# Kernel tuning notes

Measured on AMD Instinct MI355X. Metric: run time of the kernel, lower is better.

## Reference

```python
import jax, jax.numpy as jnp
import numpy as np

B, P, K = 32, 2048, 20   # events, points per event, kNN neighbors
EPS = 1e-5               # BatchNorm eps (eval mode, running stats)


def setup_inputs() -> dict:
    key = jax.random.key(0)
    ks = iter(jax.random.split(key, 64))
    inp = {}
    inp["x"] = jax.random.normal(next(ks), (B * P, 7), jnp.float32)
    inp["batch"] = jnp.repeat(jnp.arange(B, dtype=jnp.int32), P)

    def add_layer(tag, cin, cout):
        inp["w" + tag] = jax.random.normal(next(ks), (cin, cout), jnp.float32) / np.sqrt(cin)
        inp["b" + tag] = jax.random.normal(next(ks), (cout,), jnp.float32) * 0.01
        inp["g" + tag] = jax.random.uniform(next(ks), (cout,), jnp.float32, 0.5, 1.5)
        inp["e" + tag] = jax.random.normal(next(ks), (cout,), jnp.float32) * 0.1
        inp["m" + tag] = jax.random.normal(next(ks), (cout,), jnp.float32) * 0.1
        inp["v" + tag] = jax.random.uniform(next(ks), (cout,), jnp.float32, 0.5, 1.5)

    # conv1 MLP: [14, 64, 64, 64]
    add_layer("10", 14, 64)
    add_layer("11", 64, 64)
    add_layer("12", 64, 64)
    # conv2 MLP: [128, 128]
    add_layer("20", 128, 128)
    return inp


def _lin_relu_bn(h, W, b, g, be, rm, rv):
    # Linear -> ReLU -> BatchNorm1d (eval mode: running stats)
    h = jax.nn.relu(h @ W + b)
    return (h - rm) * (g / jnp.sqrt(rv + EPS)) + be


def _knn_idx(x):
    # x: [B, P, C] -> indices of K nearest neighbors (incl. self), [B, P, K]
    sq = jnp.sum(x * x, axis=-1)                                   # [B, P]
    d = sq[:, :, None] + sq[:, None, :] - 2.0 * jnp.einsum("bpc,bqc->bpq", x, x)
    _, idx = jax.lax.top_k(-d, K)
    return idx


def _edge_conv(x, mlp):
    # DynamicEdgeConv: kNN graph on current features, edge MLP([x_i, x_j - x_i]), max-aggr
    idx = _knn_idx(x)                                              # [B, P, K]
    xj = jax.vmap(lambda xb, ib: xb[ib])(x, idx)                   # [B, P, K, C]
    xi = jnp.broadcast_to(x[:, :, None, :], xj.shape)
    e = jnp.concatenate([xi, xj - xi], axis=-1)                    # [B, P, K, 2C]
    return jnp.max(mlp(e), axis=2)                                 # [B, P, Cout]


def reference(x, batch,
              w10, b10, g10, e10, m10, v10,
              w11, b11, g11, e11, m11, v11,
              w12, b12, g12, e12, m12, v12,
              w20, b20, g20, e20, m20, v20):
    xb = x.reshape(B, P, -1)                                       # fixed-size events

    def mlp1(e):
        h = _lin_relu_bn(e, w10, b10, g10, e10, m10, v10)
        h = _lin_relu_bn(h, w11, b11, g11, e11, m11, v11)
        return _lin_relu_bn(h, w12, b12, g12, e12, m12, v12)

    def mlp2(e):
        return _lin_relu_bn(e, w20, b20, g20, e20, m20, v20)

    x1 = _edge_conv(xb, mlp1)                                      # [B, P, 64]
    x2 = _edge_conv(x1, mlp2)                                      # [B, P, 128]
    out = jnp.concatenate([x1, x2], axis=-1).reshape(B * P, 192)
    return out, batch
```

## Files before the change

kernel.cpp:

```cpp
#include <hip/hip_runtime.h>

#define B_EV 32
#define P_PT 2048
#define K_NN 20
#define NPTS (B_EV*P_PT)
#define EPS_BN 1e-5f
#define RINF 3.0e38f

typedef _Float16 half8 __attribute__((ext_vector_type(8)));
typedef float f32x4 __attribute__((ext_vector_type(4)));

static constexpr int oWA10=0, oWB10=448, oB10=896, oT10=960,
  oT11=5184,
  oT12=9408,
  oWA20=9472, oWB20=17664, oB20=25856, oT20=25984,
  oB11p=26048, oB12p=26112,
  oW11hi=26176, oW11lo=28224,
  oW12hi=30272, oW12lo=32320;
static constexpr size_t oIDX = 36864;
static constexpr size_t oA1  = 1347584;
static constexpr size_t oB1  = oA1 + (size_t)NPTS*64;
static constexpr size_t oV2  = oB1 + (size_t)NPTS*64;
static constexpr size_t oX1  = oV2 + (size_t)NPTS*128;
static constexpr size_t oSQ  = oX1 + (size_t)NPTS*64;
static constexpr size_t oD   = oSQ + (size_t)NPTS;
static constexpr size_t oU2  = oA1;

__global__ __launch_bounds__(128) void k_prep(
  const float* w10,const float* b10,const float* g10,const float* e10,const float* m10,const float* v10,
  const float* w11,const float* b11,const float* g11,const float* e11,const float* m11,const float* v11,
  const float* w12,const float* b12,const float* g12,const float* e12,const float* m12,const float* v12,
  const float* w20,const float* b20,const float* g20,const float* e20,const float* m20,const float* v20,
  float* ws)
{
  __shared__ float t10s[64], t11s[64];
  int c = threadIdx.x;
  if (c < 64) {
    float s0 = g10[c]*rsqrtf(v10[c]+EPS_BN);
    ws[oB10+c]=b10[c]*s0;
    float t10 = e10[c]-m10[c]*s0; ws[oT10+c]=t10; t10s[c]=t10;
    for (int i=0;i<7;i++){
      ws[oWA10+i*64+c]=(w10[i*64+c]-w10[(7+i)*64+c])*s0;
      ws[oWB10+i*64+c]=w10[(7+i)*64+c]*s0;
    }
    float s1 = g11[c]*rsqrtf(v11[c]+EPS_BN);
    float t11 = e11[c]-m11[c]*s1; ws[oT11+c]=t11; t11s[c]=t11;
    float s2 = g12[c]*rsqrtf(v12[c]+EPS_BN);
    ws[oT12+c]=e12[c]-m12[c]*s2;
  }
  __syncthreads();
  if (c < 64) {
    float s1 = g11[c]*rsqrtf(v11[c]+EPS_BN);
    _Float16* W1hi = (_Float16*)(ws + oW11hi);
    _Float16* W1lo = (_Float16*)(ws + oW11lo);
    float acc = b11[c]*s1;
    for (int i=0;i<64;i++){
      float wv = w11[i*64+c]*s1;
      _Float16 h = (_Float16)wv;
      W1hi[c*64+i] = h;
      W1lo[c*64+i] = (_Float16)(wv - (float)h);
      acc = fmaf(t10s[i], wv, acc);
    }
    ws[oB11p+c]=acc;
    float s2 = g12[c]*rsqrtf(v12[c]+EPS_BN);
    _Float16* W2hi = (_Float16*)(ws + oW12hi);
    _Float16* W2lo = (_Float16*)(ws + oW12lo);
    float acc2 = b12[c]*s2;
    for (int i=0;i<64;i++){
      float wv = w12[i*64+c]*s2;
      _Float16 h = (_Float16)wv;
      W2hi[c*64+i] = h;
      W2lo[c*64+i] = (_Float16)(wv - (float)h);
      acc2 = fmaf(t11s[i], wv, acc2);
    }
    ws[oB12p+c]=acc2;
  }
  {
    float s = g20[c]*rsqrtf(v20[c]+EPS_BN);
    ws[oB20+c]=b20[c]*s; ws[oT20+c]=e20[c]-m20[c]*s;
    for (int i=0;i<64;i++){
      ws[oWA20+i*128+c]=(w20[i*128+c]-w20[(64+i)*128+c])*s;
      ws[oWB20+i*128+c]=w20[(64+i)*128+c]*s;
    }
  }
}

__device__ __forceinline__ void select20(float (&d)[32], int lane, int base, int g,
                                         int* __restrict__ idxout)
{
  float g4[4];
  #pragma unroll
  for (int k=0;k<4;k++){
    float m = d[8*k];
    #pragma unroll
    for (int j=1;j<8;j++) m = fminf(m, d[8*k+j]);
    g4[k]=m;
  }
  float T = 0.f;
  #pragma unroll 1
  for (int pass=0; pass<20; ++pass){
    float m = fminf(fminf(g4[0],g4[1]), fminf(g4[2],g4[3]));
    #pragma unroll
    for (int off=32; off>0; off>>=1) m = fminf(m, __shfl_xor(m, off, 64));
    if (pass==19){ T=m; break; }
    #pragma unroll
    for (int k=0;k<4;k++){
      if (g4[k]==m){
        #pragma unroll
        for (int j=0;j<8;j++) d[8*k+j] = (d[8*k+j]==m) ? RINF : d[8*k+j];
        float mm = d[8*k];
        #pragma unroll
        for (int j=1;j<8;j++) mm = fminf(mm, d[8*k+j]);
        g4[k]=mm;
      }
    }
  }
  int cnt=0;
  #pragma unroll
  for (int j=0;j<32;j++){
    bool take = (d[j]>=RINF) || (d[j]==T);
    unsigned long long mb = __ballot(take);
    if (take){
      int pos = cnt + (int)__popcll(mb & ((1ull<<lane)-1ull));
      if (pos < K_NN) idxout[(size_t)g*K_NN + pos] = base + j*64 + lane;
    }
    cnt += (int)__popcll(mb);
  }
  if (lane==0){
    for (int r=cnt; r<K_NN; ++r) idxout[(size_t)g*K_NN + r] = g;
  }
}

__global__ __launch_bounds__(1024, 8) void k_knn1(const float* __restrict__ x, int* __restrict__ idxout)
{
  __shared__ float xs[P_PT*8];
  int t = threadIdx.x;
  int b = blockIdx.x;
  int xcd = b & 7, kk = b >> 3;
  int e = xcd + ((kk >> 7) << 3);
  int blk = kk & 127;
  {
    const float* xe = x + (size_t)e*P_PT*7;
    #pragma unroll
    for (int u=0; u<2; u++){
      int p = t + u*1024;
      float v0=xe[p*7+0], v1=xe[p*7+1], v2=xe[p*7+2], v3=xe[p*7+3];
      float v4=xe[p*7+4], v5=xe[p*7+5], v6=xe[p*7+6];
      int s = (p&7)<<2;
      int w0 = (p*8) ^ s;
      int w1 = (p*8+4) ^ s;
      f32x4 lo = {v0,v1,v2,v3};
      f32x4 hi = {v4,v5,v6,0.f};
      *(f32x4*)(xs + w0) = lo;
      *(f32x4*)(xs + w1) = hi;
    }
  }
  __syncthreads();
  int lane = t & 63;
  int g = e*P_PT + blk*16 + (t>>6);
  int pin = g & (P_PT-1);
  float xp[7];
  {
    int s = (pin&7)<<2;
    f32x4 lo = *(const f32x4*)(xs + ((pin*8)^s));
    f32x4 hi = *(const f32x4*)(xs + ((pin*8+4)^s));
    xp[0]=lo[0]; xp[1]=lo[1]; xp[2]=lo[2]; xp[3]=lo[3];
    xp[4]=hi[0]; xp[5]=hi[1]; xp[6]=hi[2];
  }
  int sl = (lane&7)<<2;
  const float* base0 = xs + ((lane*8)^sl);
  const float* base1 = xs + ((lane*8+4)^sl);
  float d[32];
  #pragma unroll
  for (int j=0;j<32;j++){
    f32x4 lo = *(const f32x4*)(base0 + j*512);
    f32x4 hi = *(const f32x4*)(base1 + j*512);
    float s=0.f, df;
    df = xp[0]-lo[0]; s=fmaf(df,df,s);
    df = xp[1]-lo[1]; s=fmaf(df,df,s);
    df = xp[2]-lo[2]; s=fmaf(df,df,s);
    df = xp[3]-lo[3]; s=fmaf(df,df,s);
    df = xp[4]-hi[0]; s=fmaf(df,df,s);
    df = xp[5]-hi[1]; s=fmaf(df,df,s);
    df = xp[6]-hi[2]; s=fmaf(df,df,s);
    d[j]=s;
  }
  select20(d, lane, e*P_PT, g, idxout);
}

__global__ __launch_bounds__(256) void k_ab1(const float* __restrict__ x, const float* __restrict__ W,
                                             float* __restrict__ A1, float* __restrict__ B1)
{
  int g = blockIdx.x*256+threadIdx.x;
  float xi[7];
  #pragma unroll
  for (int i=0;i<7;i++) xi[i]=x[(size_t)g*7+i];
  float a[64], b[64];
  #pragma unroll
  for (int c=0;c<64;c++){ a[c]=W[oB10+c]; b[c]=0.f; }
  #pragma unroll
  for (int i=0;i<7;i++){
    #pragma unroll
    for (int c=0;c<64;c++) a[c]=fmaf(xi[i], W[oWA10+i*64+c], a[c]);
    #pragma unroll
    for (int c=0;c<64;c++) b[c]=fmaf(xi[i], W[oWB10+i*64+c], b[c]);
  }
  #pragma unroll
  for (int c=0;c<64;c+=4){
    float4 oa; oa.x=a[c]; oa.y=a[c+1]; oa.z=a[c+2]; oa.w=a[c+3];
    *(float4*)(A1+(size_t)g*64+c)=oa;
    float4 ob; ob.x=b[c]; ob.y=b[c+1]; ob.z=b[c+2]; ob.w=b[c+3];
    *(float4*)(B1+(size_t)g*64+c)=ob;
  }
}

__global__ __launch_bounds__(256, 2) void k_ec1m(const int* __restrict__ idx, const float* __restrict__ ws,
    const float* __restrict__ A1, const float* __restrict__ B1,
    float* __restrict__ x1, float* __restrict__ sqv, float* __restrict__ out)
{
  __shared__ float h2s[4][48*64];
  int t = threadIdx.x, w = t>>6, lane = t&63;
  int b = blockIdx.x;
  int xcd = b & 7, kk = b >> 3;
  int ev = xcd + ((kk >> 8) << 3);
  int iA = ev*P_PT + (kk & 255)*8 + w*2;
  int iB = iA + 1;
  int lg = lane>>4, lr = lane&15;

  int jT0 = idx[(size_t)iA*K_NN + lr];
  int jT1 = idx[(size_t)iB*K_NN + lr];
  int a2 = (lr < 4) ? iA*K_NN + 16 + lr : iB*K_NN + 12 + lr;
  a2 = (lr < 8) ? a2 : 0;
  int jT2 = (lr < 8) ? idx[a2] : iA;

  const float* ApA = A1 + (size_t)iA*64;
  const float* ApB = A1 + (size_t)iB*64;
  float4 avA[2][2], avB[2][2], bv[3][2][2];
  const float* Bp0 = B1 + (size_t)jT0*64;
  const float* Bp1 = B1 + (size_t)jT1*64;
  const float* Bp2 = B1 + (size_t)jT2*64;
  #pragma unroll
  for (int ks=0;ks<2;ks++){
    int c0 = ks*32 + lg*8;
    avA[ks][0] = *(const float4*)(ApA+c0); avA[ks][1] = *(const float4*)(ApA+c0+4);
    avB[ks][0] = *(const float4*)(ApB+c0); avB[ks][1] = *(const float4*)(ApB+c0+4);
    bv[0][ks][0] = *(const float4*)(Bp0+c0); bv[0][ks][1] = *(const float4*)(Bp0+c0+4);
    bv[1][ks][0] = *(const float4*)(Bp1+c0); bv[1][ks][1] = *(const float4*)(Bp1+c0+4);
    bv[2][ks][0] = *(const float4*)(Bp2+c0); bv[2][ks][1] = *(const float4*)(Bp2+c0+4);
  }

  bool useB2 = (lr >= 4) && (lr < 8);
  half8 AH[3][2], AL[3][2];
  #pragma unroll
  for (int tile=0;tile<3;tile++){
    #pragma unroll
    for (int ks=0;ks<2;ks++){
      float4 a0, a1;
      if (tile==0){ a0 = avA[ks][0]; a1 = avA[ks][1]; }
      else if (tile==1){ a0 = avB[ks][0]; a1 = avB[ks][1]; }
      else {
        a0.x = useB2 ? avB[ks][0].x : avA[ks][0].x;  a0.y = useB2 ? avB[ks][0].y : avA[ks][0].y;
        a0.z = useB2 ? avB[ks][0].z : avA[ks][0].z;  a0.w = useB2 ? avB[ks][0].w : avA[ks][0].w;
        a1.x = useB2 ? avB[ks][1].x : avA[ks][1].x;  a1.y = useB2 ? avB[ks][1].y : avA[ks][1].y;
        a1.z = useB2 ? avB[ks][1].z : avA[ks][1].z;  a1.w = useB2 ? avB[ks][1].w : avA[ks][1].w;
      }
      float hv[8];
      hv[0]=fmaxf(a0.x+bv[tile][ks][0].x,0.f); hv[1]=fmaxf(a0.y+bv[tile][ks][0].y,0.f);
      hv[2]=fmaxf(a0.z+bv[tile][ks][0].z,0.f); hv[3]=fmaxf(a0.w+bv[tile][ks][0].w,0.f);
      hv[4]=fmaxf(a1.x+bv[tile][ks][1].x,0.f); hv[5]=fmaxf(a1.y+bv[tile][ks][1].y,0.f);
      hv[6]=fmaxf(a1.z+bv[tile][ks][1].z,0.f); hv[7]=fmaxf(a1.w+bv[tile][ks][1].w,0.f);
      half8 ah, al;
      #pragma unroll
      for (int q=0;q<8;q++){
        _Float16 h = (_Float16)hv[q];
        ah[q]=h; al[q]=(_Float16)(hv[q]-(float)h);
      }
      AH[tile][ks]=ah; AL[tile][ks]=al;
    }
  }

  f32x4 acc[3][4];
  #pragma unroll
  for (int nt=0;nt<4;nt++){
    float bb = ws[oB11p + nt*16 + lr];
    f32x4 v = {bb,bb,bb,bb};
    acc[0][nt]=v; acc[1][nt]=v; acc[2][nt]=v;
  }
  {
    const _Float16* W1hi = (const _Float16*)(ws + oW11hi);
    const _Float16* W1lo = (const _Float16*)(ws + oW11lo);
    #pragma unroll
    for (int nt=0;nt<4;nt++){
      const _Float16* whp = W1hi + (nt*16+lr)*64 + lg*8;
      const _Float16* wlp = W1lo + (nt*16+lr)*64 + lg*8;
      half8 wh0 = *(const half8*)(whp);
      half8 wh1 = *(const half8*)(whp+32);
      half8 wl0 = *(const half8*)(wlp);
      half8 wl1 = *(const half8*)(wlp+32);
      #pragma unroll
      for (int tile=0;tile<3;tile++){
        acc[tile][nt] = __builtin_amdgcn_mfma_f32_16x16x32_f16(AH[tile][0], wh0, acc[tile][nt], 0,0,0);
        acc[tile][nt] = __builtin_amdgcn_mfma_f32_16x16x32_f16(AL[tile][0], wh0, acc[tile][nt], 0,0,0);
        acc[tile][nt] = __builtin_amdgcn_mfma_f32_16x16x32_f16(AH[tile][0], wl0, acc[tile][nt], 0,0,0);
        acc[tile][nt] = __builtin_amdgcn_mfma_f32_16x16x32_f16(AH[tile][1], wh1, acc[tile][nt], 0,0,0);
        acc[tile][nt] = __builtin_amdgcn_mfma_f32_16x16x32_f16(AL[tile][1], wh1, acc[tile][nt], 0,0,0);
        acc[tile][nt] = __builtin_amdgcn_mfma_f32_16x16x32_f16(AH[tile][1], wl1, acc[tile][nt], 0,0,0);
      }
    }
  }

  float* hb = h2s[w];
  #pragma unroll
  for (int tile=0;tile<3;tile++){
    #pragma unroll
    for (int nt=0;nt<4;nt++){
      #pragma unroll
      for (int r=0;r<4;r++){
        int row = tile*16 + lg*4 + r;
        int col = nt*16 + lr;
        int baddr = (row*256 + col*4) ^ ((row&7)<<4);
        *(float*)((char*)hb + baddr) = fmaxf(acc[tile][nt][r], 0.f);
      }
    }
  }

  half8 AH2[3][2], AL2[3][2];
  #pragma unroll
  for (int tile=0;tile<3;tile++){
    #pragma unroll
    for (int ks=0;ks<2;ks++){
      int row = tile*16 + lr;
      int byte0 = (row*256 + (ks*32 + lg*8)*4);
      int s = (row&7)<<4;
      f32x4 v0 = *(const f32x4*)((char*)hb + ((byte0)^s));
      f32x4 v1 = *(const f32x4*)((char*)hb + ((byte0+16)^s));
      half8 ah, al;
      #pragma unroll
      for (int q=0;q<4;q++){
        _Float16 h = (_Float16)v0[q];
        ah[q]=h; al[q]=(_Float16)(v0[q]-(float)h);
      }
      #pragma unroll
      for (int q=0;q<4;q++){
        _Float16 h = (_Float16)v1[q];
        ah[4+q]=h; al[4+q]=(_Float16)(v1[q]-(float)h);
      }
      AH2[tile][ks]=ah; AL2[tile][ks]=al;
    }
  }

  f32x4 acc2[3][4];
  #pragma unroll
  for (int nt=0;nt<4;nt++){
    float bb = ws[oB12p + nt*16 + lr];
    f32x4 v = {bb,bb,bb,bb};
    acc2[0][nt]=v; acc2[1][nt]=v; acc2[2][nt]=v;
  }
  {
    const _Float16* W2hi = (const _Float16*)(ws + oW12hi);
    const _Float16* W2lo = (const _Float16*)(ws + oW12lo);
    #pragma unroll
    for (int nt=0;nt<4;nt++){
      const _Float16* whp = W2hi + (nt*16+lr)*64 + lg*8;
      const _Float16* wlp = W2lo + (nt*16+lr)*64 + lg*8;
      half8 wh0 = *(const half8*)(whp);
      half8 wh1 = *(const half8*)(whp+32);
      half8 wl0 = *(const half8*)(wlp);
      half8 wl1 = *(const half8*)(wlp+32);
      #pragma unroll
      for (int tile=0;tile<3;tile++){
        acc2[tile][nt] = __builtin_amdgcn_mfma_f32_16x16x32_f16(AH2[tile][0], wh0, acc2[tile][nt], 0,0,0);
        acc2[tile][nt] = __builtin_amdgcn_mfma_f32_16x16x32_f16(AL2[tile][0], wh0, acc2[tile][nt], 0,0,0);
        acc2[tile][nt] = __builtin_amdgcn_mfma_f32_16x16x32_f16(AH2[tile][0], wl0, acc2[tile][nt], 0,0,0);
        acc2[tile][nt] = __builtin_amdgcn_mfma_f32_16x16x32_f16(AH2[tile][1], wh1, acc2[tile][nt], 0,0,0);
        acc2[tile][nt] = __builtin_amdgcn_mfma_f32_16x16x32_f16(AL2[tile][1], wh1, acc2[tile][nt], 0,0,0);
        acc2[tile][nt] = __builtin_amdgcn_mfma_f32_16x16x32_f16(AH2[tile][1], wl1, acc2[tile][nt], 0,0,0);
      }
    }
  }

  float finA[4], finB[4];
  float sqA = 0.f, sqB = 0.f;
  #pragma unroll
  for (int nt=0;nt<4;nt++){
    float cvA = -RINF;
    #pragma unroll
    for (int r=0;r<4;r++) cvA = fmaxf(cvA, acc2[0][nt][r]);
    if (lg==0){
      #pragma unroll
      for (int r=0;r<4;r++) cvA = fmaxf(cvA, acc2[2][nt][r]);
    }
    cvA = fmaxf(cvA, __shfl_xor(cvA,16,64));
    cvA = fmaxf(cvA, __shfl_xor(cvA,32,64));
    finA[nt] = fmaxf(cvA, 0.f) + ws[oT12 + nt*16 + lr];
    sqA = fmaf(finA[nt], finA[nt], sqA);

    float cvB = -RINF;
    #pragma unroll
    for (int r=0;r<4;r++) cvB = fmaxf(cvB, acc2[1][nt][r]);
    if (lg==1){
      #pragma unroll
      for (int r=0;r<4;r++) cvB = fmaxf(cvB, acc2[2][nt][r]);
    }
    cvB = fmaxf(cvB, __shfl_xor(cvB,16,64));
    cvB = fmaxf(cvB, __shfl_xor(cvB,32,64));
    finB[nt] = fmaxf(cvB, 0.f) + ws[oT12 + nt*16 + lr];
    sqB = fmaf(finB[nt], finB[nt], sqB);
  }
  if (lane < 16){
    #pragma unroll
    for (int nt=0;nt<4;nt++){
      x1[(size_t)iA*64 + nt*16 + lane] = finA[nt];
      out[(size_t)iA*192 + nt*16 + lane] = finA[nt];
      x1[(size_t)iB*64 + nt*16 + lane] = finB[nt];
      out[(size_t)iB*192 + nt*16 + lane] = finB[nt];
    }
  }
  #pragma unroll
  for (int off=1; off<16; off<<=1){
    sqA += __shfl_xor(sqA, off, 64);
    sqB += __shfl_xor(sqB, off, 64);
  }
  if (lane == 0){ sqv[iA] = sqA; sqv[iB] = sqB; }
}

__global__ __launch_bounds__(256) void k_dist2(const float* __restrict__ x1, const float* __restrict__ sqv,
                                               float* __restrict__ D, int e0, int ce)
{
  __shared__ float As[64][68], Bs[64][68];
  int b = blockIdx.x;
  int z, inner;
  if (ce == 8){ z = b & 7; inner = b >> 3; }
  else        { z = b / 1024; inner = b % 1024; }
  int by = inner >> 5, bx = inner & 31;
  int e = e0 + z;
  const float* Xe = x1 + (size_t)e*P_PT*64;
  int rb = by*64, cb = bx*64;
  int t = threadIdx.x;
  int tr = t>>4, tk=(t&15)*4;
  #pragma unroll
  for (int rr=0;rr<4;rr++){
    int r = tr + 16*rr;
    float4 va = *(const float4*)(Xe + (size_t)(rb+r)*64 + tk);
    As[tk][r]=va.x; As[tk+1][r]=va.y; As[tk+2][r]=va.z; As[tk+3][r]=va.w;
    float4 vb = *(const float4*)(Xe + (size_t)(cb+r)*64 + tk);
    Bs[tk][r]=vb.x; Bs[tk+1][r]=vb.y; Bs[tk+2][r]=vb.z; Bs[tk+3][r]=vb.w;
  }
  __syncthreads();
  int tx=t&15, ty=t>>4;
  float acc[4][4];
  #pragma unroll
  for (int i=0;i<4;i++){
    #pragma unroll
    for (int j=0;j<4;j++) acc[i][j]=0.f;
  }
  #pragma unroll 4
  for (int k=0;k<64;k++){
    float4 a4 = *(const float4*)(&As[k][ty*4]);
    float4 b4 = *(const float4*)(&Bs[k][tx*4]);
    float a0=a4.x, a1=a4.y, a2=a4.z, a3=a4.w;
    float b0=b4.x, b1=b4.y, b2=b4.z, b3=b4.w;
    acc[0][0]=fmaf(a0,b0,acc[0][0]); acc[0][1]=fmaf(a0,b1,acc[0][1]);
    acc[0][2]=fmaf(a0,b2,acc[0][2]); acc[0][3]=fmaf(a0,b3,acc[0][3]);
    acc[1][0]=fmaf(a1,b0,acc[1][0]); acc[1][1]=fmaf(a1,b1,acc[1][1]);
    acc[1][2]=fmaf(a1,b2,acc[1][2]); acc[1][3]=fmaf(a1,b3,acc[1][3]);
    acc[2][0]=fmaf(a2,b0,acc[2][0]); acc[2][1]=fmaf(a2,b1,acc[2][1]);
    acc[2][2]=fmaf(a2,b2,acc[2][2]); acc[2][3]=fmaf(a2,b3,acc[2][3]);
    acc[3][0]=fmaf(a3,b0,acc[3][0]); acc[3][1]=fmaf(a3,b1,acc[3][1]);
    acc[3][2]=fmaf(a3,b2,acc[3][2]); acc[3][3]=fmaf(a3,b3,acc[3][3]);
  }
  float sr[4], sc[4];
  #pragma unroll
  for (int i=0;i<4;i++){ sr[i]=sqv[e*P_PT + rb+ty*4+i]; sc[i]=sqv[e*P_PT + cb+tx*4+i]; }
  #pragma unroll
  for (int i=0;i<4;i++){
    float4 o;
    o.x = sr[i]+sc[0]-2.f*acc[i][0];
    o.y = sr[i]+sc[1]-2.f*acc[i][1];
    o.z = sr[i]+sc[2]-2.f*acc[i][2];
    o.w = sr[i]+sc[3]-2.f*acc[i][3];
    *(float4*)(D + (size_t)(z*P_PT + rb+ty*4+i)*P_PT + cb + tx*4) = o;
  }
}

__global__ __launch_bounds__(256) void k_sel2(const float* __restrict__ D, int* __restrict__ idxout, int e0)
{
  int t=threadIdx.x, lane=t&63;
  int pl = blockIdx.x*4 + (t>>6);
  int le = pl>>11, pin = pl&(P_PT-1);
  int e = e0 + le;
  int g = e*P_PT + pin;
  const float* Dr = D + (size_t)pl*P_PT;
  float d[32];
  #pragma unroll
  for (int j=0;j<32;j++) d[j]=Dr[j*64+lane];
  select20(d, lane, e*P_PT, g, idxout);
}

__global__ __launch_bounds__(256) void k_uv2(const float* __restrict__ x1, const float* __restrict__ W,
                                             float* __restrict__ U2, float* __restrict__ V2)
{
  int g = blockIdx.x*256 + threadIdx.x;
  int half = blockIdx.y & 1;
  bool isU = blockIdx.y < 2;
  const float* Wb = W + (isU?oWA20:oWB20) + half*64;
  float acc[64];
  #pragma unroll
  for (int c=0;c<64;c++) acc[c] = isU ? W[oB20+half*64+c] : 0.f;
  const float* xp = x1 + (size_t)g*64;
  #pragma unroll 1
  for (int i=0;i<64;i+=4){
    float4 xv = *(const float4*)(xp+i);
    #pragma unroll
    for (int c=0;c<64;c++) acc[c]=fmaf(xv.x, Wb[(i+0)*128+c], acc[c]);
    #pragma unroll
    for (int c=0;c<64;c++) acc[c]=fmaf(xv.y, Wb[(i+1)*128+c], acc[c]);
    #pragma unroll
    for (int c=0;c<64;c++) acc[c]=fmaf(xv.z, Wb[(i+2)*128+c], acc[c]);
    #pragma unroll
    for (int c=0;c<64;c++) acc[c]=fmaf(xv.w, Wb[(i+3)*128+c], acc[c]);
  }
  float* dst = (isU?U2:V2) + (size_t)g*128 + half*64;
  #pragma unroll
  for (int c=0;c<64;c+=4){
    float4 o; o.x=acc[c]; o.y=acc[c+1]; o.z=acc[c+2]; o.w=acc[c+3];
    *(float4*)(dst+c)=o;
  }
}

__global__ __launch_bounds__(256) void k_gather2(const int* __restrict__ idx, const float* __restrict__ U2,
     const float* __restrict__ V2, const float* __restrict__ W, float* __restrict__ out)
{
  int b = blockIdx.x;
  int xcd = b & 7, kk = b >> 3;
  int ev = xcd + ((kk >> 3) << 3);
  int g = ev*P_PT + (kk & 7)*256 + threadIdx.x;
  int half = blockIdx.y;
  float mx[64];
  #pragma unroll
  for (int c=0;c<64;c++) mx[c]=-RINF;
  for (int k=0;k<K_NN;k++){
    int j = idx[(size_t)g*K_NN+k];
    const float4* vp = (const float4*)(V2 + (size_t)j*128 + half*64);
    #pragma unroll
    for (int c4=0;c4<16;c4++){
      float4 v=vp[c4];
      mx[c4*4+0]=fmaxf(mx[c4*4+0],v.x);
      mx[c4*4+1]=fmaxf(mx[c4*4+1],v.y);
      mx[c4*4+2]=fmaxf(mx[c4*4+2],v.z);
      mx[c4*4+3]=fmaxf(mx[c4*4+3],v.w);
    }
  }
  const float* Up = U2 + (size_t)g*128 + half*64;
  float* op = out + (size_t)g*192 + 64 + half*64;
  #pragma unroll
  for (int c=0;c<64;c+=4){
    float4 o;
    o.x = fmaxf(Up[c+0]+mx[c+0],0.f)+W[oT20+half*64+c+0];
    o.y = fmaxf(Up[c+1]+mx[c+1],0.f)+W[oT20+half*64+c+1];
    o.z = fmaxf(Up[c+2]+mx[c+2],0.f)+W[oT20+half*64+c+2];
    o.w = fmaxf(Up[c+3]+mx[c+3],0.f)+W[oT20+half*64+c+3];
    *(float4*)(op+c)=o;
  }
}

__global__ __launch_bounds__(256) void k_batchf(const int* __restrict__ batch, float* __restrict__ out){
  int i = blockIdx.x*256+threadIdx.x;
  out[(size_t)NPTS*192 + i] = (float)batch[i];
}

extern "C" void kernel_launch(void* const* d_in, const int* in_sizes, int n_in,
                              void* d_out, int out_size, void* d_ws, size_t ws_size,
                              hipStream_t stream)
{
  const float* x     = (const float*)d_in[0];
  const int*   batch = (const int*)d_in[1];
  const float* w10=(const float*)d_in[2],  *b10=(const float*)d_in[3],  *g10=(const float*)d_in[4],
             *e10=(const float*)d_in[5],  *m10=(const float*)d_in[6],  *v10=(const float*)d_in[7];
  const float* w11=(const float*)d_in[8],  *b11=(const float*)d_in[9],  *g11=(const float*)d_in[10],
             *e11=(const float*)d_in[11], *m11=(const float*)d_in[12], *v11=(const float*)d_in[13];
  const float* w12=(const float*)d_in[14], *b12=(const float*)d_in[15], *g12=(const float*)d_in[16],
             *e12=(const float*)d_in[17], *m12=(const float*)d_in[18], *v12=(const float*)d_in[19];
  const float* w20=(const float*)d_in[20], *b20=(const float*)d_in[21], *g20=(const float*)d_in[22],
             *e20=(const float*)d_in[23], *m20=(const float*)d_in[24], *v20=(const float*)d_in[25];

  float* ws  = (float*)d_ws;
  float* out = (float*)d_out;
  int*   idxp = (int*)(ws + oIDX);

  k_prep<<<1,128,0,stream>>>(w10,b10,g10,e10,m10,v10, w11,b11,g11,e11,m11,v11,
                             w12,b12,g12,e12,m12,v12, w20,b20,g20,e20,m20,v20, ws);
  k_knn1<<<NPTS/16, 1024, 0, stream>>>(x, idxp);
  k_ab1<<<NPTS/256, 256, 0, stream>>>(x, ws, ws+oA1, ws+oB1);
  k_ec1m<<<NPTS/8, 256, 0, stream>>>(idxp, ws, ws+oA1, ws+oB1, ws+oX1, ws+oSQ, out);

  size_t wsFloats = ws_size/4;
  long avail = (long)wsFloats - (long)oD;
  int CE = (int)(avail / (2048L*2048L));
  if (CE < 1) CE = 1;
  if (CE > 8) CE = 8;
  for (int e0=0; e0<B_EV; e0+=CE){
    int ce = (B_EV - e0 < CE) ? (B_EV - e0) : CE;
    k_dist2<<<ce*1024,256,0,stream>>>(ws+oX1, ws+oSQ, ws+oD, e0, ce);
    k_sel2<<<ce*512,256,0,stream>>>(ws+oD, idxp, e0);
  }

  k_uv2<<<dim3(NPTS/256,4),256,0,stream>>>(ws+oX1, ws, ws+oU2, ws+oV2);
  k_gather2<<<dim3(NPTS/256,2),256,0,stream>>>(idxp, ws+oU2, ws+oV2, ws, out);
  k_batchf<<<NPTS/256,256,0,stream>>>(batch, out);
}
```

Measured before the change: 1.002 ms.

## Fuse second-stage kNN distance and top-k selection into one MFMA kernel

Replaces the chunked k_dist2/k_sel2 pair, which wrote full 2048x2048 distance matrices per event to global memory and read them back, with one fused kernel. Each block computes distances for 16 query points against all points of the event using f16 MFMA, with a hi/lo split (four MFMAs) to recover near-fp32 accuracy, stages tiles through shared memory and selects top-20 in registers. The batch-to-float output write is folded into k_gather2 to save a launch. This removes large global memory traffic and many launches. In exchange each block recomputes the B-side f16 conversion for every chunk, and the split-f16 dot product could reorder near-tied neighbours.

```diff
diff --git a/kernel.cpp b/kernel.cpp
--- a/kernel.cpp
+++ b/kernel.cpp
@@ -23,7 +23,6 @@
 static constexpr size_t oV2  = oB1 + (size_t)NPTS*64;
 static constexpr size_t oX1  = oV2 + (size_t)NPTS*128;
 static constexpr size_t oSQ  = oX1 + (size_t)NPTS*64;
-static constexpr size_t oD   = oSQ + (size_t)NPTS;
 static constexpr size_t oU2  = oA1;
 
 __global__ __launch_bounds__(128) void k_prep(
@@ -424,77 +423,72 @@
   if (lane == 0){ sqv[iA] = sqA; sqv[iB] = sqB; }
 }
 
-__global__ __launch_bounds__(256) void k_dist2(const float* __restrict__ x1, const float* __restrict__ sqv,
-                                               float* __restrict__ D, int e0, int ce)
-{
-  __shared__ float As[64][68], Bs[64][68];
+__global__ __launch_bounds__(1024, 4) void k_dsel(const float* __restrict__ x1,
+    const float* __restrict__ sqv, int* __restrict__ idxout)
+{
+  __shared__ float cs[16][260];
+  int t = threadIdx.x, w = t>>6, lane = t&63;
   int b = blockIdx.x;
-  int z, inner;
-  if (ce == 8){ z = b & 7; inner = b >> 3; }
-  else        { z = b / 1024; inner = b % 1024; }
-  int by = inner >> 5, bx = inner & 31;
-  int e = e0 + z;
+  int xcd = b & 7, kk = b >> 3;
+  int e = xcd + ((kk >> 7) << 3);
+  int base16 = e*P_PT + (kk & 127)*16;
+  int lg = lane>>4, lr = lane&15;
+
+  half8 AH[2], AL[2];
+  {
+    const float* Ap = x1 + (size_t)(base16 + lr)*64;
+    #pragma unroll
+    for (int kx=0;kx<2;kx++){
+      float4 a0 = *(const float4*)(Ap + kx*32 + lg*8);
+      float4 a1 = *(const float4*)(Ap + kx*32 + lg*8 + 4);
+      float hv[8] = {a0.x,a0.y,a0.z,a0.w,a1.x,a1.y,a1.z,a1.w};
+      half8 ah, al;
+      #pragma unroll
+      for (int q=0;q<8;q++){
+        _Float16 h = (_Float16)hv[q];
+        ah[q]=h; al[q]=(_Float16)(hv[q]-(float)h);
+      }
+      AH[kx]=ah; AL[kx]=al;
+    }
+  }
+  int p = base16 + w;
+  float sqp = sqv[p];
   const float* Xe = x1 + (size_t)e*P_PT*64;
-  int rb = by*64, cb = bx*64;
-  int t = threadIdx.x;
-  int tr = t>>4, tk=(t&15)*4;
-  #pragma unroll
-  for (int rr=0;rr<4;rr++){
-    int r = tr + 16*rr;
-    float4 va = *(const float4*)(Xe + (size_t)(rb+r)*64 + tk);
-    As[tk][r]=va.x; As[tk+1][r]=va.y; As[tk+2][r]=va.z; As[tk+3][r]=va.w;
-    float4 vb = *(const float4*)(Xe + (size_t)(cb+r)*64 + tk);
-    Bs[tk][r]=vb.x; Bs[tk+1][r]=vb.y; Bs[tk+2][r]=vb.z; Bs[tk+3][r]=vb.w;
-  }
-  __syncthreads();
-  int tx=t&15, ty=t>>4;
-  float acc[4][4];
-  #pragma unroll
-  for (int i=0;i<4;i++){
-    #pragma unroll
-    for (int j=0;j<4;j++) acc[i][j]=0.f;
-  }
-  #pragma unroll 4
-  for (int k=0;k<64;k++){
-    float4 a4 = *(const float4*)(&As[k][ty*4]);
-    float4 b4 = *(const float4*)(&Bs[k][tx*4]);
-    float a0=a4.x, a1=a4.y, a2=a4.z, a3=a4.w;
-    float b0=b4.x, b1=b4.y, b2=b4.z, b3=b4.w;
-    acc[0][0]=fmaf(a0,b0,acc[0][0]); acc[0][1]=fmaf(a0,b1,acc[0][1]);
-    acc[0][2]=fmaf(a0,b2,acc[0][2]); acc[0][3]=fmaf(a0,b3,acc[0][3]);
-    acc[1][0]=fmaf(a1,b0,acc[1][0]); acc[1][1]=fmaf(a1,b1,acc[1][1]);
-    acc[1][2]=fmaf(a1,b2,acc[1][2]); acc[1][3]=fmaf(a1,b3,acc[1][3]);
-    acc[2][0]=fmaf(a2,b0,acc[2][0]); acc[2][1]=fmaf(a2,b1,acc[2][1]);
-    acc[2][2]=fmaf(a2,b2,acc[2][2]); acc[2][3]=fmaf(a2,b3,acc[2][3]);
-    acc[3][0]=fmaf(a3,b0,acc[3][0]); acc[3][1]=fmaf(a3,b1,acc[3][1]);
-    acc[3][2]=fmaf(a3,b2,acc[3][2]); acc[3][3]=fmaf(a3,b3,acc[3][3]);
-  }
-  float sr[4], sc[4];
-  #pragma unroll
-  for (int i=0;i<4;i++){ sr[i]=sqv[e*P_PT + rb+ty*4+i]; sc[i]=sqv[e*P_PT + cb+tx*4+i]; }
-  #pragma unroll
-  for (int i=0;i<4;i++){
-    float4 o;
-    o.x = sr[i]+sc[0]-2.f*acc[i][0];
-    o.y = sr[i]+sc[1]-2.f*acc[i][1];
-    o.z = sr[i]+sc[2]-2.f*acc[i][2];
-    o.w = sr[i]+sc[3]-2.f*acc[i][3];
-    *(float4*)(D + (size_t)(z*P_PT + rb+ty*4+i)*P_PT + cb + tx*4) = o;
-  }
-}
-
-__global__ __launch_bounds__(256) void k_sel2(const float* __restrict__ D, int* __restrict__ idxout, int e0)
-{
-  int t=threadIdx.x, lane=t&63;
-  int pl = blockIdx.x*4 + (t>>6);
-  int le = pl>>11, pin = pl&(P_PT-1);
-  int e = e0 + le;
-  int g = e*P_PT + pin;
-  const float* Dr = D + (size_t)pl*P_PT;
+  const float* sqe = sqv + e*P_PT;
+
   float d[32];
-  #pragma unroll
-  for (int j=0;j<32;j++) d[j]=Dr[j*64+lane];
-  select20(d, lane, e*P_PT, g, idxout);
+  #pragma unroll 1
+  for (int chunk=0; chunk<8; ++chunk){
+    int c = chunk*256 + w*16 + lr;
+    const float* Bp = Xe + (size_t)c*64;
+    f32x4 acc = {0.f,0.f,0.f,0.f};
+    #pragma unroll
+    for (int kx=0;kx<2;kx++){
+      float4 b0 = *(const float4*)(Bp + kx*32 + lg*8);
+      float4 b1 = *(const float4*)(Bp + kx*32 + lg*8 + 4);
+      float hv[8] = {b0.x,b0.y,b0.z,b0.w,b1.x,b1.y,b1.z,b1.w};
+      half8 bh, bl;
+      #pragma unroll
+      for (int q=0;q<8;q++){
+        _Float16 h = (_Float16)hv[q];
+        bh[q]=h; bl[q]=(_Float16)(hv[q]-(float)h);
+      }
+      acc = __builtin_amdgcn_mfma_f32_16x16x32_f16(AH[kx], bh, acc, 0,0,0);
+      acc = __builtin_amdgcn_mfma_f32_16x16x32_f16(AL[kx], bh, acc, 0,0,0);
+      acc = __builtin_amdgcn_mfma_f32_16x16x32_f16(AH[kx], bl, acc, 0,0,0);
+      acc = __builtin_amdgcn_mfma_f32_16x16x32_f16(AL[kx], bl, acc, 0,0,0);
+    }
+    #pragma unroll
+    for (int r=0;r<4;r++) cs[4*lg + r][w*16 + lr] = acc[r];
+    __syncthreads();
+    #pragma unroll
+    for (int jj=0;jj<4;jj++){
+      float sqc = sqe[chunk*256 + jj*64 + lane];
+      d[chunk*4 + jj] = sqp + sqc - 2.f*cs[w][jj*64 + lane];
+    }
+    __syncthreads();
+  }
+  select20(d, lane, e*P_PT, p, idxout);
 }
 
 __global__ __launch_bounds__(256) void k_uv2(const float* __restrict__ x1, const float* __restrict__ W,
@@ -529,13 +523,15 @@
 }
 
 __global__ __launch_bounds__(256) void k_gather2(const int* __restrict__ idx, const float* __restrict__ U2,
-     const float* __restrict__ V2, const float* __restrict__ W, float* __restrict__ out)
+     const float* __restrict__ V2, const float* __restrict__ W, const int* __restrict__ batch,
+     float* __restrict__ out)
 {
   int b = blockIdx.x;
   int xcd = b & 7, kk = b >> 3;
   int ev = xcd + ((kk >> 3) << 3);
   int g = ev*P_PT + (kk & 7)*256 + threadIdx.x;
   int half = blockIdx.y;
+  if (half == 0) out[(size_t)NPTS*192 + g] = (float)batch[g];
   float mx[64];
   #pragma unroll
   for (int c=0;c<64;c++) mx[c]=-RINF;
@@ -562,11 +558,6 @@
     o.w = fmaxf(Up[c+3]+mx[c+3],0.f)+W[oT20+half*64+c+3];
     *(float4*)(op+c)=o;
   }
-}
-
-__global__ __launch_bounds__(256) void k_batchf(const int* __restrict__ batch, float* __restrict__ out){
-  int i = blockIdx.x*256+threadIdx.x;
-  out[(size_t)NPTS*192 + i] = (float)batch[i];
 }
 
 extern "C" void kernel_launch(void* const* d_in, const int* in_sizes, int n_in,
@@ -593,19 +584,7 @@
   k_knn1<<<NPTS/16, 1024, 0, stream>>>(x, idxp);
   k_ab1<<<NPTS/256, 256, 0, stream>>>(x, ws, ws+oA1, ws+oB1);
   k_ec1m<<<NPTS/8, 256, 0, stream>>>(idxp, ws, ws+oA1, ws+oB1, ws+oX1, ws+oSQ, out);
-
-  size_t wsFloats = ws_size/4;
-  long avail = (long)wsFloats - (long)oD;
-  int CE = (int)(avail / (2048L*2048L));
-  if (CE < 1) CE = 1;
-  if (CE > 8) CE = 8;
-  for (int e0=0; e0<B_EV; e0+=CE){
-    int ce = (B_EV - e0 < CE) ? (B_EV - e0) : CE;
-    k_dist2<<<ce*1024,256,0,stream>>>(ws+oX1, ws+oSQ, ws+oD, e0, ce);
-    k_sel2<<<ce*512,256,0,stream>>>(ws+oD, idxp, e0);
-  }
-
+  k_dsel<<<NPTS/16, 1024, 0, stream>>>(ws+oX1, ws+oSQ, idxp);
   k_uv2<<<dim3(NPTS/256,4),256,0,stream>>>(ws+oX1, ws, ws+oU2, ws+oV2);
-  k_gather2<<<dim3(NPTS/256,2),256,0,stream>>>(idxp, ws+oU2, ws+oV2, ws, out);
-  k_batchf<<<NPTS/256,256,0,stream>>>(batch, out);
-}
+  k_gather2<<<dim3(NPTS/256,2),256,0,stream>>>(idxp, ws+oU2, ws+oV2, ws, batch, out);
+}
```

Measured after the change: 1.096 ms. 1.09x slower.
